# Kernel optimization log

Measured on AMD Instinct MI355X. Metric: run time of the kernel, lower is better.

The kernel has to match this reference:

```python
import jax, jax.numpy as jnp
import numpy as np

B, N, E = 4, 8192, 65536
OBS, H, OUT, NOUT = 128, 256, 1024, 18


def setup_inputs() -> dict:
    key = jax.random.key(0)
    ks = jax.random.split(key, 8)
    nodes = jax.random.normal(ks[0], (B, N, OBS), dtype=jnp.float32)
    edges = jax.random.randint(ks[1], (B, 2, E), 0, N, dtype=jnp.int64)
    # Glorot-ish init for weights
    W0 = jax.random.normal(ks[2], (OBS, H), dtype=jnp.float32) / np.float32(np.sqrt(OBS))
    W1 = jax.random.normal(ks[3], (H, OUT), dtype=jnp.float32) / np.float32(np.sqrt(H))
    W_logit = jax.random.normal(ks[4], (OUT, NOUT), dtype=jnp.float32) / np.float32(np.sqrt(OUT))
    W_val = jax.random.normal(ks[5], (OUT, 1), dtype=jnp.float32) / np.float32(np.sqrt(OUT))
    return {
        "nodes": nodes, "edges": edges,
        "W0": W0, "b0": jnp.zeros((H,), jnp.float32),
        "W1": W1, "b1": jnp.zeros((OUT,), jnp.float32),
        "W_logit": W_logit, "b_logit": jnp.zeros((NOUT,), jnp.float32),
        "W_val": W_val, "b_val": jnp.zeros((1,), jnp.float32),
    }


def _gcn_layer(x, src, dst, W, b, n):
    # PyG GCNConv: out = D^{-1/2} (A + I) D^{-1/2} X W + b   (self-loops already in src/dst)
    h = x @ W                                                     # [N, F_out]
    deg = jax.ops.segment_sum(jnp.ones(src.shape, jnp.float32), dst, num_segments=n)
    dinv = jnp.where(deg > 0, jax.lax.rsqrt(deg), 0.0)            # deg^{-1/2}
    norm = dinv[src] * dinv[dst]                                  # [Etot]
    msg = h[src] * norm[:, None]                                  # gather + normalize
    agg = jax.ops.segment_sum(msg, dst, num_segments=n)           # scatter-add
    return agg + b


def reference(nodes, edges, W0, b0, W1, b1, W_logit, b_logit, W_val, b_val):
    n = nodes.shape[1]
    loops = jnp.arange(n, dtype=edges.dtype)  # self-loops, added by GCNConv

    def per_graph(x, ei):
        src = jnp.concatenate([ei[0], loops])
        dst = jnp.concatenate([ei[1], loops])
        h = jax.nn.relu(_gcn_layer(x, src, dst, W0, b0, n))
        # (original applies F.dropout here; omitted for a deterministic reference)
        h = jax.nn.relu(_gcn_layer(h, src, dst, W1, b1, n))
        return h

    out = jax.vmap(per_graph)(nodes, edges)        # [B, N, OUT]
    logits = out @ W_logit + b_logit               # [B, N, NOUT]
    values = (out @ W_val + b_val)[..., 0]         # [B, N]
    return logits, values
```

## Files before the change

kernel.cpp:

```cpp
#include <hip/hip_runtime.h>
#include <hip/hip_bf16.h>

#define BB   4
#define NN   8192
#define EE   65536
#define FOBS 128
#define FH   256
#define FOUT 1024
#define NLOG 18
#define BKT  64

typedef __attribute__((ext_vector_type(8))) short frag8;
typedef __attribute__((ext_vector_type(4))) float f32x4;

__device__ __forceinline__ ushort f2b(float v) {
    __hip_bfloat16 h = __float2bfloat16(v);
    return *reinterpret_cast<ushort*>(&h);
}
__device__ __forceinline__ float blo(uint u) { return __uint_as_float(u << 16); }
__device__ __forceinline__ float bhi(uint u) { return __uint_as_float(u & 0xffff0000u); }

__device__ __forceinline__ void gld16(const void* g, void* l) {
    __builtin_amdgcn_global_load_lds(
        (const __attribute__((address_space(1))) unsigned*)g,
        (__attribute__((address_space(3))) unsigned*)l, 16, 0, 0);
}

#define W0_N   (FOBS * FH)
#define W1_N   (FH * FOUT)
#define WH_N   (19 * FOUT)
#define CUR_N  (BB * NN)
#define OUTI_N (BB * NN * 19)
#define PREP_TOTAL (W0_N + W1_N + WH_N + CUR_N + OUTI_N)

__global__ void prep_kernel(const float* __restrict__ W0, ushort* __restrict__ W0T,
                            const float* __restrict__ W1, ushort* __restrict__ W1T,
                            const float* __restrict__ Wl, const float* __restrict__ Wv,
                            ushort* __restrict__ WT19, int* __restrict__ cursor,
                            const float* __restrict__ bl, const float* __restrict__ bv,
                            float* __restrict__ out_logits, float* __restrict__ out_values) {
    int idx = blockIdx.x * blockDim.x + threadIdx.x;
    if (idx < W0_N) {
        int n = idx / FOBS, k = idx - n * FOBS;
        W0T[idx] = f2b(W0[(size_t)k * FH + n]);
        return;
    }
    idx -= W0_N;
    if (idx < W1_N) {
        int n = idx / FH, k = idx - n * FH;
        W1T[idx] = f2b(W1[(size_t)k * FOUT + n]);
        return;
    }
    idx -= W1_N;
    if (idx < WH_N) {
        int o = idx >> 10, k = idx & (FOUT - 1);
        WT19[idx] = f2b((o < NLOG) ? Wl[(size_t)k * NLOG + o] : Wv[k]);
        return;
    }
    idx -= WH_N;
    if (idx < CUR_N) { cursor[idx] = 0; return; }
    idx -= CUR_N;
    if (idx < OUTI_N) {
        int gn = idx / 19, o = idx - gn * 19;
        if (o < NLOG) out_logits[(size_t)gn * NLOG + o] = bl[o];
        else          out_values[gn] = bv[0];
    }
}

__global__ void bucket_fill(const int* __restrict__ edges, int* __restrict__ cursor,
                            int* __restrict__ bucket) {
    int blk = blockIdx.x;
    int xcd = blk & 7;
    int g = xcd >> 1;
    int chunk = (blk >> 3) * 2 + (xcd & 1);
    int e = chunk * 256 + threadIdx.x;
    const int* src = edges + (size_t)g * 2 * EE;
    const int* dst = src + EE;
    int d = dst[e];
    int slot = atomicAdd(&cursor[(size_t)g * NN + d], 1);
    if (slot < BKT) bucket[((size_t)g * NN + d) * BKT + slot] = src[e];
}

__global__ __launch_bounds__(256) void gather_agg_f32(
    const float* __restrict__ x_all, const int* __restrict__ cnt_all,
    const int* __restrict__ bucket, uint* __restrict__ agg_all)
{
    int blk = blockIdx.x;
    int xcd = blk & 7;
    int g = xcd >> 1;
    int chunk = (blk >> 3) * 2 + (xcd & 1);
    int wv = threadIdx.x >> 6, lane = threadIdx.x & 63;
    int n = chunk * 4 + wv;
    const float2* x = (const float2*)(x_all + (size_t)g * NN * FOBS);
    const int* cnt = cnt_all + (size_t)g * NN;
    const int* bkt = bucket + ((size_t)g * NN + n) * BKT;

    int cn = cnt[n];
    float wn = rsqrtf((float)cn + 1.0f);
    int deg = min(cn, BKT);

    float2 self = x[(size_t)n * 64 + lane];
    float ax = wn * wn * self.x, ay = wn * wn * self.y;

    for (int i = 0; i < deg; i += 8) {
        int last = deg - 1;
        int s0 = bkt[i];
        int s1 = bkt[min(i + 1, last)], s2 = bkt[min(i + 2, last)], s3 = bkt[min(i + 3, last)];
        int s4 = bkt[min(i + 4, last)], s5 = bkt[min(i + 5, last)], s6 = bkt[min(i + 6, last)];
        int s7 = bkt[min(i + 7, last)];
        float w0 = rsqrtf((float)cnt[s0] + 1.0f) * wn;
        float w1 = (i + 1 < deg) ? rsqrtf((float)cnt[s1] + 1.0f) * wn : 0.0f;
        float w2 = (i + 2 < deg) ? rsqrtf((float)cnt[s2] + 1.0f) * wn : 0.0f;
        float w3 = (i + 3 < deg) ? rsqrtf((float)cnt[s3] + 1.0f) * wn : 0.0f;
        float w4 = (i + 4 < deg) ? rsqrtf((float)cnt[s4] + 1.0f) * wn : 0.0f;
        float w5 = (i + 5 < deg) ? rsqrtf((float)cnt[s5] + 1.0f) * wn : 0.0f;
        float w6 = (i + 6 < deg) ? rsqrtf((float)cnt[s6] + 1.0f) * wn : 0.0f;
        float w7 = (i + 7 < deg) ? rsqrtf((float)cnt[s7] + 1.0f) * wn : 0.0f;
        float2 r0 = x[(size_t)s0 * 64 + lane], r1 = x[(size_t)s1 * 64 + lane];
        float2 r2 = x[(size_t)s2 * 64 + lane], r3 = x[(size_t)s3 * 64 + lane];
        float2 r4 = x[(size_t)s4 * 64 + lane], r5 = x[(size_t)s5 * 64 + lane];
        float2 r6 = x[(size_t)s6 * 64 + lane], r7 = x[(size_t)s7 * 64 + lane];
        ax += w0 * r0.x + w1 * r1.x + w2 * r2.x + w3 * r3.x
            + w4 * r4.x + w5 * r5.x + w6 * r6.x + w7 * r7.x;
        ay += w0 * r0.y + w1 * r1.y + w2 * r2.y + w3 * r3.y
            + w4 * r4.y + w5 * r5.y + w6 * r6.y + w7 * r7.y;
    }
    agg_all[((size_t)g * NN + n) * 64 + lane] = (uint)f2b(ax) | ((uint)f2b(ay) << 16);
}

__global__ __launch_bounds__(256) void gather_agg_b256(
    const uint2* __restrict__ xb_all, const int* __restrict__ cnt_all,
    const int* __restrict__ bucket, uint2* __restrict__ agg_all)
{
    int blk = blockIdx.x;
    int xcd = blk & 7;
    int g = xcd >> 1;
    int chunk = (blk >> 3) * 2 + (xcd & 1);
    int wv = threadIdx.x >> 6, lane = threadIdx.x & 63;
    int n = chunk * 4 + wv;
    const uint2* xb = xb_all + (size_t)g * NN * 64;
    const int* cnt = cnt_all + (size_t)g * NN;
    const int* bkt = bucket + ((size_t)g * NN + n) * BKT;

    int cn = cnt[n];
    float wn = rsqrtf((float)cn + 1.0f);
    int deg = min(cn, BKT);

    uint2 u = xb[(size_t)n * 64 + lane];
    float w2s = wn * wn;
    float a0 = w2s * blo(u.x), a1 = w2s * bhi(u.x), a2 = w2s * blo(u.y), a3 = w2s * bhi(u.y);

    for (int i = 0; i < deg; i += 8) {
        int last = deg - 1;
        int s0 = bkt[i];
        int s1 = bkt[min(i + 1, last)], s2 = bkt[min(i + 2, last)], s3 = bkt[min(i + 3, last)];
        int s4 = bkt[min(i + 4, last)], s5 = bkt[min(i + 5, last)], s6 = bkt[min(i + 6, last)];
        int s7 = bkt[min(i + 7, last)];
        float w0 = rsqrtf((float)cnt[s0] + 1.0f) * wn;
        float w1 = (i + 1 < deg) ? rsqrtf((float)cnt[s1] + 1.0f) * wn : 0.0f;
        float w2 = (i + 2 < deg) ? rsqrtf((float)cnt[s2] + 1.0f) * wn : 0.0f;
        float w3 = (i + 3 < deg) ? rsqrtf((float)cnt[s3] + 1.0f) * wn : 0.0f;
        float w4 = (i + 4 < deg) ? rsqrtf((float)cnt[s4] + 1.0f) * wn : 0.0f;
        float w5 = (i + 5 < deg) ? rsqrtf((float)cnt[s5] + 1.0f) * wn : 0.0f;
        float w6 = (i + 6 < deg) ? rsqrtf((float)cnt[s6] + 1.0f) * wn : 0.0f;
        float w7 = (i + 7 < deg) ? rsqrtf((float)cnt[s7] + 1.0f) * wn : 0.0f;
        uint2 r0 = xb[(size_t)s0 * 64 + lane], r1 = xb[(size_t)s1 * 64 + lane];
        uint2 r2 = xb[(size_t)s2 * 64 + lane], r3 = xb[(size_t)s3 * 64 + lane];
        uint2 r4 = xb[(size_t)s4 * 64 + lane], r5 = xb[(size_t)s5 * 64 + lane];
        uint2 r6 = xb[(size_t)s6 * 64 + lane], r7 = xb[(size_t)s7 * 64 + lane];
        a0 += w0 * blo(r0.x) + w1 * blo(r1.x) + w2 * blo(r2.x) + w3 * blo(r3.x)
            + w4 * blo(r4.x) + w5 * blo(r5.x) + w6 * blo(r6.x) + w7 * blo(r7.x);
        a1 += w0 * bhi(r0.x) + w1 * bhi(r1.x) + w2 * bhi(r2.x) + w3 * bhi(r3.x)
            + w4 * bhi(r4.x) + w5 * bhi(r5.x) + w6 * bhi(r6.x) + w7 * bhi(r7.x);
        a2 += w0 * blo(r0.y) + w1 * blo(r1.y) + w2 * blo(r2.y) + w3 * blo(r3.y)
            + w4 * blo(r4.y) + w5 * blo(r5.y) + w6 * blo(r6.y) + w7 * blo(r7.y);
        a3 += w0 * bhi(r0.y) + w1 * bhi(r1.y) + w2 * bhi(r2.y) + w3 * bhi(r3.y)
            + w4 * bhi(r4.y) + w5 * bhi(r5.y) + w6 * bhi(r6.y) + w7 * bhi(r7.y);
    }
    uint2 o;
    o.x = (uint)f2b(a0) | ((uint)f2b(a1) << 16);
    o.y = (uint)f2b(a2) | ((uint)f2b(a3) << 16);
    agg_all[((size_t)g * NN + n) * 64 + lane] = o;
}

__global__ __launch_bounds__(256) void mfma_gemm(
    const ushort* __restrict__ A_all, const ushort* __restrict__ BT,
    const float* __restrict__ bias, ushort* __restrict__ C_all,
    int M, int N, int K, int relu)
{
    __shared__ __align__(16) ushort As[128 * 64];
    __shared__ __align__(16) ushort Bs[128 * 64];

    int g = blockIdx.z;
    const ushort* A = A_all + (size_t)g * M * K;
    ushort* C = C_all + (size_t)g * M * N;

    int t = threadIdx.x;
    int bn = blockIdx.x, bm = blockIdx.y;
    int lane = t & 63, w = t >> 6;
    int wm = w >> 1, wn = w & 1;
    int l15 = lane & 15, quad = lane >> 4;

    f32x4 acc[4][4] = {};

    const char* Abase = (const char*)(A + (size_t)(bm * 128) * K);
    const char* Bbase = (const char*)(BT + (size_t)(bn * 128) * K);
    size_t rstride = (size_t)K * 2;

    int rsub = lane >> 3;
    int colb = (lane & 7) * 16;

    for (int k0 = 0; k0 < K; k0 += 64) {
#pragma unroll
        for (int c = 0; c < 4; ++c) {
            int grp = c * 4 + w;
            int row = grp * 8 + rsub;
            int gcol = k0 * 2 + (colb ^ ((row & 7) << 4));
            gld16(Abase + (size_t)row * rstride + gcol, (char*)As + grp * 1024);
            gld16(Bbase + (size_t)row * rstride + gcol, (char*)Bs + grp * 1024);
        }
        __syncthreads();
#pragma unroll
        for (int kk = 0; kk < 64; kk += 32) {
            frag8 af[4], bf[4];
#pragma unroll
            for (int i = 0; i < 4; ++i) {
                int r = wm * 64 + i * 16 + l15;
                int cb = (kk * 2 + quad * 16) ^ ((r & 7) << 4);
                af[i] = *(const frag8*)((const char*)As + r * 128 + cb);
            }
#pragma unroll
            for (int j = 0; j < 4; ++j) {
                int r = wn * 64 + j * 16 + l15;
                int cb = (kk * 2 + quad * 16) ^ ((r & 7) << 4);
                bf[j] = *(const frag8*)((const char*)Bs + r * 128 + cb);
            }
#pragma unroll
            for (int i = 0; i < 4; ++i)
#pragma unroll
                for (int j = 0; j < 4; ++j)
                    acc[i][j] = __builtin_amdgcn_mfma_f32_16x16x32_bf16(af[i], bf[j], acc[i][j], 0, 0, 0);
        }
        __syncthreads();
    }

#pragma unroll
    for (int i = 0; i < 4; ++i) {
#pragma unroll
        for (int j = 0; j < 4; ++j) {
            int col = bn * 128 + wn * 64 + j * 16 + l15;
            float bcol = bias[col];
#pragma unroll
            for (int r = 0; r < 4; ++r) {
                int row = bm * 128 + wm * 64 + i * 16 + quad * 4 + r;
                float v = acc[i][j][r] + bcol;
                if (relu) v = fmaxf(v, 0.0f);
                C[(size_t)row * N + col] = f2b(v);
            }
        }
    }
}

__global__ __launch_bounds__(256) void gemm2_heads(
    const ushort* __restrict__ hagg_all,
    const ushort* __restrict__ W1T,
    const float*  __restrict__ b1,
    const ushort* __restrict__ WT19,
    float* __restrict__ out_logits,
    float* __restrict__ out_values)
{
    __shared__ __align__(16) ushort smem[128 * 136];
    __shared__ __align__(16) ushort wt[20][136];

    char* AsB = (char*)smem;
    char* BsB = (char*)smem + 16384;
    ushort* Ct = smem;

    int bm = blockIdx.x, sp = blockIdx.y, g = blockIdx.z;
    int t = threadIdx.x;
    int lane = t & 63, w = t >> 6;
    int wm = w >> 1, wn = w & 1;
    int l15 = lane & 15, quad = lane >> 4;

    const char* A0 = (const char*)(hagg_all + ((size_t)g * NN + bm * 128) * FH);

    if (t < 136) wt[19][t] = 0;

    int rsub = lane >> 3;
    int colb = (lane & 7) * 16;

    f32x4 hacc[2][2] = {};

    for (int bi = 0; bi < 4; ++bi) {
        int bn = sp * 4 + bi;
        __syncthreads();

        for (int idx = t; idx < 19 * 16; idx += 256) {
            int row = idx >> 4, c8 = (idx & 15) * 8;
            *(uint4*)&wt[row][c8] = *(const uint4*)(WT19 + (size_t)row * FOUT + bn * 128 + c8);
        }

        f32x4 acc[4][4] = {};
        const char* Bbase = (const char*)(W1T + (size_t)(bn * 128) * FH);

        for (int k0 = 0; k0 < FH; k0 += 64) {
#pragma unroll
            for (int c = 0; c < 4; ++c) {
                int grp = c * 4 + w;
                int row = grp * 8 + rsub;
                int gcol = k0 * 2 + (colb ^ ((row & 7) << 4));
                gld16(A0 + (size_t)row * (FH * 2) + gcol, AsB + grp * 1024);
                gld16(Bbase + (size_t)row * (FH * 2) + gcol, BsB + grp * 1024);
            }
            __syncthreads();
#pragma unroll
            for (int kk = 0; kk < 64; kk += 32) {
                frag8 af[4], bf[4];
#pragma unroll
                for (int i = 0; i < 4; ++i) {
                    int r = wm * 64 + i * 16 + l15;
                    int cb = (kk * 2 + quad * 16) ^ ((r & 7) << 4);
                    af[i] = *(const frag8*)(AsB + r * 128 + cb);
                }
#pragma unroll
                for (int j = 0; j < 4; ++j) {
                    int r = wn * 64 + j * 16 + l15;
                    int cb = (kk * 2 + quad * 16) ^ ((r & 7) << 4);
                    bf[j] = *(const frag8*)(BsB + r * 128 + cb);
                }
#pragma unroll
                for (int i = 0; i < 4; ++i)
#pragma unroll
                    for (int j = 0; j < 4; ++j)
                        acc[i][j] = __builtin_amdgcn_mfma_f32_16x16x32_bf16(af[i], bf[j], acc[i][j], 0, 0, 0);
            }
            __syncthreads();
        }

#pragma unroll
        for (int j = 0; j < 4; ++j) {
            int colL = wn * 64 + j * 16 + l15;
            float bcol = b1[bn * 128 + colL];
#pragma unroll
            for (int i = 0; i < 4; ++i) {
                int rowL = wm * 64 + i * 16 + quad * 4;
#pragma unroll
                for (int r = 0; r < 4; ++r) {
                    float v = fmaxf(acc[i][j][r] + bcol, 0.0f);
                    Ct[(size_t)(rowL + r) * 136 + colL] = f2b(v);
                }
            }
        }
        __syncthreads();

        int r1 = (l15 < 3) ? (16 + l15) : 19;
#pragma unroll
        for (int kk = 0; kk < 128; kk += 32) {
            frag8 b0 = *(const frag8*)&wt[l15][kk + quad * 8];
            frag8 bO = *(const frag8*)&wt[r1][kk + quad * 8];
#pragma unroll
            for (int mt = 0; mt < 2; ++mt) {
                int row = (w * 2 + mt) * 16 + l15;
                frag8 af = *(const frag8*)&Ct[(size_t)row * 136 + kk + quad * 8];
                hacc[mt][0] = __builtin_amdgcn_mfma_f32_16x16x32_bf16(af, b0, hacc[mt][0], 0, 0, 0);
                hacc[mt][1] = __builtin_amdgcn_mfma_f32_16x16x32_bf16(af, bO, hacc[mt][1], 0, 0, 0);
            }
        }
    }

#pragma unroll
    for (int mt = 0; mt < 2; ++mt) {
#pragma unroll
        for (int r = 0; r < 4; ++r) {
            int node = bm * 128 + (w * 2 + mt) * 16 + quad * 4 + r;
            size_t gn = (size_t)g * NN + node;
            atomicAdd(&out_logits[gn * NLOG + l15], hacc[mt][0][r]);
            if (l15 < 2)       atomicAdd(&out_logits[gn * NLOG + 16 + l15], hacc[mt][1][r]);
            else if (l15 == 2) atomicAdd(&out_values[gn], hacc[mt][1][r]);
        }
    }
}

extern "C" void kernel_launch(void* const* d_in, const int* in_sizes, int n_in,
                              void* d_out, int out_size, void* d_ws, size_t ws_size,
                              hipStream_t stream) {
    const float* nodes = (const float*)d_in[0];
    const int*   edges = (const int*)d_in[1];
    const float* W0 = (const float*)d_in[2];
    const float* b0 = (const float*)d_in[3];
    const float* W1 = (const float*)d_in[4];
    const float* b1 = (const float*)d_in[5];
    const float* Wl = (const float*)d_in[6];
    const float* bl = (const float*)d_in[7];
    const float* Wv = (const float*)d_in[8];
    const float* bv = (const float*)d_in[9];

    float* out_logits = (float*)d_out;
    float* out_values = out_logits + (size_t)BB * NN * NLOG;

    char* ws = (char*)d_ws;
    int*    cursor  = (int*)(ws);
    ushort* W0T     = (ushort*)(ws + (128 << 10));
    ushort* W1T     = (ushort*)(ws + (192 << 10));
    ushort* WT19    = (ushort*)(ws + (704 << 10));
    int*    bucket  = (int*)(ws + (1u << 20));
    ushort* xagg_b  = (ushort*)(ws + (9u << 20));
    ushort* h1b     = (ushort*)(ws + (17u << 20));
    ushort* hagg_b  = (ushort*)(ws + (33u << 20));

    prep_kernel<<<(PREP_TOTAL + 255) / 256, 256, 0, stream>>>(
        W0, W0T, W1, W1T, Wl, Wv, WT19, cursor, bl, bv, out_logits, out_values);

    bucket_fill<<<1024, 256, 0, stream>>>(edges, cursor, bucket);

    gather_agg_f32<<<(NN / 4) * BB, 256, 0, stream>>>(nodes, cursor, bucket, (uint*)xagg_b);

    mfma_gemm<<<dim3(FH / 128, NN / 128, BB), 256, 0, stream>>>(
        xagg_b, W0T, b0, h1b, NN, FH, FOBS, 1);

    gather_agg_b256<<<(NN / 4) * BB, 256, 0, stream>>>((const uint2*)h1b, cursor, bucket,
                                                       (uint2*)hagg_b);

    gemm2_heads<<<dim3(NN / 128, 2, BB), 256, 0, stream>>>(hagg_b, W1T, b1, WT19,
                                                           out_logits, out_values);
}
```

Measured before the change: 187.5 us.

## Restructure head GEMM to full-width blocks with resident A panel and direct stores

The fused GEMM2+heads kernel now runs one 512-thread block per 128-row tile covering all 1024 output columns. It keeps the whole A panel in LDS and double-buffers W1 tiles, prefetching the next one while the current one is used. Because each block owns its rows completely, head outputs are written directly with bias added, replacing atomicAdd and the bias pre-initialisation in the prep kernel. The gather kernels also load bucket indices as two int4 vectors instead of eight scalar loads. In exchange the grid is halved, and the larger LDS footprint (about 135 KB) likely allows only one block per CU.

```diff
diff --git a/kernel.cpp b/kernel.cpp
--- a/kernel.cpp
+++ b/kernel.cpp
@@ -30,15 +30,12 @@
 #define W1_N   (FH * FOUT)
 #define WH_N   (19 * FOUT)
 #define CUR_N  (BB * NN)
-#define OUTI_N (BB * NN * 19)
-#define PREP_TOTAL (W0_N + W1_N + WH_N + CUR_N + OUTI_N)
+#define PREP_TOTAL (W0_N + W1_N + WH_N + CUR_N)
 
 __global__ void prep_kernel(const float* __restrict__ W0, ushort* __restrict__ W0T,
                             const float* __restrict__ W1, ushort* __restrict__ W1T,
                             const float* __restrict__ Wl, const float* __restrict__ Wv,
-                            ushort* __restrict__ WT19, int* __restrict__ cursor,
-                            const float* __restrict__ bl, const float* __restrict__ bv,
-                            float* __restrict__ out_logits, float* __restrict__ out_values) {
+                            ushort* __restrict__ WT19, int* __restrict__ cursor) {
     int idx = blockIdx.x * blockDim.x + threadIdx.x;
     if (idx < W0_N) {
         int n = idx / FOBS, k = idx - n * FOBS;
@@ -58,13 +55,7 @@
         return;
     }
     idx -= WH_N;
-    if (idx < CUR_N) { cursor[idx] = 0; return; }
-    idx -= CUR_N;
-    if (idx < OUTI_N) {
-        int gn = idx / 19, o = idx - gn * 19;
-        if (o < NLOG) out_logits[(size_t)gn * NLOG + o] = bl[o];
-        else          out_values[gn] = bv[0];
-    }
+    if (idx < CUR_N) cursor[idx] = 0;
 }
 
 __global__ void bucket_fill(const int* __restrict__ edges, int* __restrict__ cursor,
@@ -103,11 +94,16 @@
     float ax = wn * wn * self.x, ay = wn * wn * self.y;
 
     for (int i = 0; i < deg; i += 8) {
-        int last = deg - 1;
-        int s0 = bkt[i];
-        int s1 = bkt[min(i + 1, last)], s2 = bkt[min(i + 2, last)], s3 = bkt[min(i + 3, last)];
-        int s4 = bkt[min(i + 4, last)], s5 = bkt[min(i + 5, last)], s6 = bkt[min(i + 6, last)];
-        int s7 = bkt[min(i + 7, last)];
+        int4 va = *(const int4*)&bkt[i];
+        int4 vb = *(const int4*)&bkt[i + 4];
+        int s0 = va.x;
+        int s1 = (i + 1 < deg) ? va.y : s0;
+        int s2 = (i + 2 < deg) ? va.z : s0;
+        int s3 = (i + 3 < deg) ? va.w : s0;
+        int s4 = (i + 4 < deg) ? vb.x : s0;
+        int s5 = (i + 5 < deg) ? vb.y : s0;
+        int s6 = (i + 6 < deg) ? vb.z : s0;
+        int s7 = (i + 7 < deg) ? vb.w : s0;
         float w0 = rsqrtf((float)cnt[s0] + 1.0f) * wn;
         float w1 = (i + 1 < deg) ? rsqrtf((float)cnt[s1] + 1.0f) * wn : 0.0f;
         float w2 = (i + 2 < deg) ? rsqrtf((float)cnt[s2] + 1.0f) * wn : 0.0f;
@@ -151,11 +147,16 @@
     float a0 = w2s * blo(u.x), a1 = w2s * bhi(u.x), a2 = w2s * blo(u.y), a3 = w2s * bhi(u.y);
 
     for (int i = 0; i < deg; i += 8) {
-        int last = deg - 1;
-        int s0 = bkt[i];
-        int s1 = bkt[min(i + 1, last)], s2 = bkt[min(i + 2, last)], s3 = bkt[min(i + 3, last)];
-        int s4 = bkt[min(i + 4, last)], s5 = bkt[min(i + 5, last)], s6 = bkt[min(i + 6, last)];
-        int s7 = bkt[min(i + 7, last)];
+        int4 va = *(const int4*)&bkt[i];
+        int4 vb = *(const int4*)&bkt[i + 4];
+        int s0 = va.x;
+        int s1 = (i + 1 < deg) ? va.y : s0;
+        int s2 = (i + 2 < deg) ? va.z : s0;
+        int s3 = (i + 3 < deg) ? va.w : s0;
+        int s4 = (i + 4 < deg) ? vb.x : s0;
+        int s5 = (i + 5 < deg) ? vb.y : s0;
+        int s6 = (i + 6 < deg) ? vb.z : s0;
+        int s7 = (i + 7 < deg) ? vb.w : s0;
         float w0 = rsqrtf((float)cnt[s0] + 1.0f) * wn;
         float w1 = (i + 1 < deg) ? rsqrtf((float)cnt[s1] + 1.0f) * wn : 0.0f;
         float w2 = (i + 2 < deg) ? rsqrtf((float)cnt[s2] + 1.0f) * wn : 0.0f;
@@ -261,85 +262,103 @@
     }
 }
 
-__global__ __launch_bounds__(256) void gemm2_heads(
+__global__ __launch_bounds__(512) void gemm2_heads(
     const ushort* __restrict__ hagg_all,
     const ushort* __restrict__ W1T,
     const float*  __restrict__ b1,
     const ushort* __restrict__ WT19,
+    const float*  __restrict__ bl,
+    const float*  __restrict__ bv,
     float* __restrict__ out_logits,
     float* __restrict__ out_values)
 {
-    __shared__ __align__(16) ushort smem[128 * 136];
+    __shared__ __align__(16) char Apan[4][16384];
+    __shared__ __align__(16) char BsD[2][16384];
+    __shared__ __align__(16) ushort Ct[128 * 136];
     __shared__ __align__(16) ushort wt[20][136];
 
-    char* AsB = (char*)smem;
-    char* BsB = (char*)smem + 16384;
-    ushort* Ct = smem;
-
-    int bm = blockIdx.x, sp = blockIdx.y, g = blockIdx.z;
+    int bm = blockIdx.x, g = blockIdx.y;
     int t = threadIdx.x;
     int lane = t & 63, w = t >> 6;
-    int wm = w >> 1, wn = w & 1;
+    int wm = w >> 2, wn = w & 3;
     int l15 = lane & 15, quad = lane >> 4;
-
-    const char* A0 = (const char*)(hagg_all + ((size_t)g * NN + bm * 128) * FH);
-
-    if (t < 136) wt[19][t] = 0;
-
     int rsub = lane >> 3;
     int colb = (lane & 7) * 16;
 
-    f32x4 hacc[2][2] = {};
-
-    for (int bi = 0; bi < 4; ++bi) {
-        int bn = sp * 4 + bi;
-        __syncthreads();
-
-        for (int idx = t; idx < 19 * 16; idx += 256) {
-            int row = idx >> 4, c8 = (idx & 15) * 8;
-            *(uint4*)&wt[row][c8] = *(const uint4*)(WT19 + (size_t)row * FOUT + bn * 128 + c8);
-        }
-
-        f32x4 acc[4][4] = {};
-        const char* Bbase = (const char*)(W1T + (size_t)(bn * 128) * FH);
-
-        for (int k0 = 0; k0 < FH; k0 += 64) {
-#pragma unroll
-            for (int c = 0; c < 4; ++c) {
-                int grp = c * 4 + w;
-                int row = grp * 8 + rsub;
-                int gcol = k0 * 2 + (colb ^ ((row & 7) << 4));
-                gld16(A0 + (size_t)row * (FH * 2) + gcol, AsB + grp * 1024);
-                gld16(Bbase + (size_t)row * (FH * 2) + gcol, BsB + grp * 1024);
-            }
-            __syncthreads();
+    const char* A0 = (const char*)(hagg_all + ((size_t)g * NN + bm * 128) * FH);
+
+#pragma unroll
+    for (int cc = 0; cc < 8; ++cc) {
+        int grp = cc * 8 + w;
+        int chunk = grp >> 4, gi = grp & 15;
+        int row = gi * 8 + rsub;
+        int gcol = chunk * 128 + (colb ^ ((row & 7) << 4));
+        gld16(A0 + (size_t)row * (FH * 2) + gcol, Apan[chunk] + gi * 1024);
+    }
+#pragma unroll
+    for (int c = 0; c < 2; ++c) {
+        int grp = c * 8 + w;
+        int row = grp * 8 + rsub;
+        int gcol = colb ^ ((row & 7) << 4);
+        gld16((const char*)W1T + (size_t)row * (FH * 2) + gcol, BsD[0] + grp * 1024);
+    }
+    if (t < 136) wt[19][t] = 0;
+    __syncthreads();
+
+    f32x4 hacc[2] = {};
+
+    for (int bn = 0; bn < 8; ++bn) {
+        f32x4 acc[4][2] = {};
+#pragma unroll
+        for (int k0i = 0; k0i < 4; ++k0i) {
+            int s = bn * 4 + k0i;
+            if (s < 31) {
+                int ns = s + 1;
+                int nbn = ns >> 2, nk = ns & 3;
+                const char* Bb = (const char*)(W1T + (size_t)(nbn * 128) * FH);
+#pragma unroll
+                for (int c = 0; c < 2; ++c) {
+                    int grp = c * 8 + w;
+                    int row = grp * 8 + rsub;
+                    int gcol = nk * 128 + (colb ^ ((row & 7) << 4));
+                    gld16(Bb + (size_t)row * (FH * 2) + gcol, BsD[ns & 1] + grp * 1024);
+                }
+            }
+            if (k0i == 0) {
+                for (int idx = t; idx < 19 * 16; idx += 512) {
+                    int row = idx >> 4, c8 = (idx & 15) * 8;
+                    *(uint4*)&wt[row][c8] = *(const uint4*)(WT19 + (size_t)row * FOUT + bn * 128 + c8);
+                }
+            }
+            const char* Bs = BsD[s & 1];
+            const char* Ap = Apan[k0i];
 #pragma unroll
             for (int kk = 0; kk < 64; kk += 32) {
-                frag8 af[4], bf[4];
+                frag8 af[4], bf[2];
 #pragma unroll
                 for (int i = 0; i < 4; ++i) {
                     int r = wm * 64 + i * 16 + l15;
                     int cb = (kk * 2 + quad * 16) ^ ((r & 7) << 4);
-                    af[i] = *(const frag8*)(AsB + r * 128 + cb);
+                    af[i] = *(const frag8*)(Ap + r * 128 + cb);
                 }
 #pragma unroll
-                for (int j = 0; j < 4; ++j) {
-                    int r = wn * 64 + j * 16 + l15;
+                for (int j = 0; j < 2; ++j) {
+                    int r = wn * 32 + j * 16 + l15;
                     int cb = (kk * 2 + quad * 16) ^ ((r & 7) << 4);
-                    bf[j] = *(const frag8*)(BsB + r * 128 + cb);
+                    bf[j] = *(const frag8*)(Bs + r * 128 + cb);
                 }
 #pragma unroll
                 for (int i = 0; i < 4; ++i)
 #pragma unroll
-                    for (int j = 0; j < 4; ++j)
+                    for (int j = 0; j < 2; ++j)
                         acc[i][j] = __builtin_amdgcn_mfma_f32_16x16x32_bf16(af[i], bf[j], acc[i][j], 0, 0, 0);
             }
             __syncthreads();
         }
 
 #pragma unroll
-        for (int j = 0; j < 4; ++j) {
-            int colL = wn * 64 + j * 16 + l15;
+        for (int j = 0; j < 2; ++j) {
+            int colL = wn * 32 + j * 16 + l15;
             float bcol = b1[bn * 128 + colL];
 #pragma unroll
             for (int i = 0; i < 4; ++i) {
@@ -358,26 +377,20 @@
         for (int kk = 0; kk < 128; kk += 32) {
             frag8 b0 = *(const frag8*)&wt[l15][kk + quad * 8];
             frag8 bO = *(const frag8*)&wt[r1][kk + quad * 8];
-#pragma unroll
-            for (int mt = 0; mt < 2; ++mt) {
-                int row = (w * 2 + mt) * 16 + l15;
-                frag8 af = *(const frag8*)&Ct[(size_t)row * 136 + kk + quad * 8];
-                hacc[mt][0] = __builtin_amdgcn_mfma_f32_16x16x32_bf16(af, b0, hacc[mt][0], 0, 0, 0);
-                hacc[mt][1] = __builtin_amdgcn_mfma_f32_16x16x32_bf16(af, bO, hacc[mt][1], 0, 0, 0);
-            }
-        }
-    }
-
-#pragma unroll
-    for (int mt = 0; mt < 2; ++mt) {
-#pragma unroll
-        for (int r = 0; r < 4; ++r) {
-            int node = bm * 128 + (w * 2 + mt) * 16 + quad * 4 + r;
-            size_t gn = (size_t)g * NN + node;
-            atomicAdd(&out_logits[gn * NLOG + l15], hacc[mt][0][r]);
-            if (l15 < 2)       atomicAdd(&out_logits[gn * NLOG + 16 + l15], hacc[mt][1][r]);
-            else if (l15 == 2) atomicAdd(&out_values[gn], hacc[mt][1][r]);
-        }
+            frag8 af = *(const frag8*)&Ct[(size_t)(w * 16 + l15) * 136 + kk + quad * 8];
+            hacc[0] = __builtin_amdgcn_mfma_f32_16x16x32_bf16(af, b0, hacc[0], 0, 0, 0);
+            hacc[1] = __builtin_amdgcn_mfma_f32_16x16x32_bf16(af, bO, hacc[1], 0, 0, 0);
+        }
+        __syncthreads();
+    }
+
+#pragma unroll
+    for (int r = 0; r < 4; ++r) {
+        int node = bm * 128 + w * 16 + quad * 4 + r;
+        size_t gn = (size_t)g * NN + node;
+        out_logits[gn * NLOG + l15] = hacc[0][r] + bl[l15];
+        if (l15 < 2)       out_logits[gn * NLOG + 16 + l15] = hacc[1][r] + bl[16 + l15];
+        else if (l15 == 2) out_values[gn] = hacc[1][r] + bv[0];
     }
 }
 
@@ -409,7 +422,7 @@
     ushort* hagg_b  = (ushort*)(ws + (33u << 20));
 
     prep_kernel<<<(PREP_TOTAL + 255) / 256, 256, 0, stream>>>(
-        W0, W0T, W1, W1T, Wl, Wv, WT19, cursor, bl, bv, out_logits, out_values);
+        W0, W0T, W1, W1T, Wl, Wv, WT19, cursor);
 
     bucket_fill<<<1024, 256, 0, stream>>>(edges, cursor, bucket);
 
@@ -421,6 +434,6 @@
     gather_agg_b256<<<(NN / 4) * BB, 256, 0, stream>>>((const uint2*)h1b, cursor, bucket,
                                                        (uint2*)hagg_b);
 
-    gemm2_heads<<<dim3(NN / 128, 2, BB), 256, 0, stream>>>(hagg_b, W1T, b1, WT19,
-                                                           out_logits, out_values);
-}
+    gemm2_heads<<<dim3(NN / 128, BB), 512, 0, stream>>>(hagg_b, W1T, b1, WT19, bl, bv,
+                                                        out_logits, out_values);
+}
```

Measured after the change: 189.7 us. Within noise of the previous version (+1.2%).

## Pre-convert node features to bf16 and store bucket indices as 16-bit

Applied to the files above, without the earlier changes.

The prep kernel now converts the fp32 node features to packed bf16, so the first gather reads half as many bytes per neighbour row. Bucket entries are stored as ushort instead of int, and both gather kernels load eight indices with one 16-byte vector load. This cuts gather traffic and index loads, at the cost of an extra full pass over the nodes in prep and bf16 rounding of the layer-1 inputs. The vector index load reads past deg, but stays inside the fixed 64-slot bucket.

```diff
diff --git a/kernel.cpp b/kernel.cpp
--- a/kernel.cpp
+++ b/kernel.cpp
@@ -26,20 +26,28 @@
         (__attribute__((address_space(3))) unsigned*)l, 16, 0, 0);
 }
 
+#define XB2_N  (BB * NN * FOBS / 2)
 #define W0_N   (FOBS * FH)
 #define W1_N   (FH * FOUT)
 #define WH_N   (19 * FOUT)
 #define CUR_N  (BB * NN)
 #define OUTI_N (BB * NN * 19)
-#define PREP_TOTAL (W0_N + W1_N + WH_N + CUR_N + OUTI_N)
-
-__global__ void prep_kernel(const float* __restrict__ W0, ushort* __restrict__ W0T,
+#define PREP_TOTAL (XB2_N + W0_N + W1_N + WH_N + CUR_N + OUTI_N)
+
+__global__ void prep_kernel(const float* __restrict__ nodes, uint* __restrict__ xb,
+                            const float* __restrict__ W0, ushort* __restrict__ W0T,
                             const float* __restrict__ W1, ushort* __restrict__ W1T,
                             const float* __restrict__ Wl, const float* __restrict__ Wv,
                             ushort* __restrict__ WT19, int* __restrict__ cursor,
                             const float* __restrict__ bl, const float* __restrict__ bv,
                             float* __restrict__ out_logits, float* __restrict__ out_values) {
     int idx = blockIdx.x * blockDim.x + threadIdx.x;
+    if (idx < XB2_N) {
+        float2 xx = ((const float2*)nodes)[idx];
+        xb[idx] = (uint)f2b(xx.x) | ((uint)f2b(xx.y) << 16);
+        return;
+    }
+    idx -= XB2_N;
     if (idx < W0_N) {
         int n = idx / FOBS, k = idx - n * FOBS;
         W0T[idx] = f2b(W0[(size_t)k * FH + n]);
@@ -68,7 +76,7 @@
 }
 
 __global__ void bucket_fill(const int* __restrict__ edges, int* __restrict__ cursor,
-                            int* __restrict__ bucket) {
+                            ushort* __restrict__ bucket) {
     int blk = blockIdx.x;
     int xcd = blk & 7;
     int g = xcd >> 1;
@@ -78,12 +86,12 @@
     const int* dst = src + EE;
     int d = dst[e];
     int slot = atomicAdd(&cursor[(size_t)g * NN + d], 1);
-    if (slot < BKT) bucket[((size_t)g * NN + d) * BKT + slot] = src[e];
-}
-
-__global__ __launch_bounds__(256) void gather_agg_f32(
-    const float* __restrict__ x_all, const int* __restrict__ cnt_all,
-    const int* __restrict__ bucket, uint* __restrict__ agg_all)
+    if (slot < BKT) bucket[((size_t)g * NN + d) * BKT + slot] = (ushort)src[e];
+}
+
+__global__ __launch_bounds__(256) void gather_agg_b128(
+    const uint* __restrict__ xb_all, const int* __restrict__ cnt_all,
+    const ushort* __restrict__ bucket, uint* __restrict__ agg_all)
 {
     int blk = blockIdx.x;
     int xcd = blk & 7;
@@ -91,23 +99,28 @@
     int chunk = (blk >> 3) * 2 + (xcd & 1);
     int wv = threadIdx.x >> 6, lane = threadIdx.x & 63;
     int n = chunk * 4 + wv;
-    const float2* x = (const float2*)(x_all + (size_t)g * NN * FOBS);
+    const uint* xb = xb_all + (size_t)g * NN * 64;
     const int* cnt = cnt_all + (size_t)g * NN;
-    const int* bkt = bucket + ((size_t)g * NN + n) * BKT;
+    const ushort* bkt = bucket + ((size_t)g * NN + n) * BKT;
 
     int cn = cnt[n];
     float wn = rsqrtf((float)cn + 1.0f);
     int deg = min(cn, BKT);
 
-    float2 self = x[(size_t)n * 64 + lane];
-    float ax = wn * wn * self.x, ay = wn * wn * self.y;
+    uint u = xb[(size_t)n * 64 + lane];
+    float w2s = wn * wn;
+    float a0 = w2s * blo(u), a1 = w2s * bhi(u);
 
     for (int i = 0; i < deg; i += 8) {
-        int last = deg - 1;
-        int s0 = bkt[i];
-        int s1 = bkt[min(i + 1, last)], s2 = bkt[min(i + 2, last)], s3 = bkt[min(i + 3, last)];
-        int s4 = bkt[min(i + 4, last)], s5 = bkt[min(i + 5, last)], s6 = bkt[min(i + 6, last)];
-        int s7 = bkt[min(i + 7, last)];
+        uint4 va = *(const uint4*)&bkt[i];
+        int s0 = (int)(va.x & 0xffffu);
+        int s1 = (i + 1 < deg) ? (int)(va.x >> 16) : s0;
+        int s2 = (i + 2 < deg) ? (int)(va.y & 0xffffu) : s0;
+        int s3 = (i + 3 < deg) ? (int)(va.y >> 16) : s0;
+        int s4 = (i + 4 < deg) ? (int)(va.z & 0xffffu) : s0;
+        int s5 = (i + 5 < deg) ? (int)(va.z >> 16) : s0;
+        int s6 = (i + 6 < deg) ? (int)(va.w & 0xffffu) : s0;
+        int s7 = (i + 7 < deg) ? (int)(va.w >> 16) : s0;
         float w0 = rsqrtf((float)cnt[s0] + 1.0f) * wn;
         float w1 = (i + 1 < deg) ? rsqrtf((float)cnt[s1] + 1.0f) * wn : 0.0f;
         float w2 = (i + 2 < deg) ? rsqrtf((float)cnt[s2] + 1.0f) * wn : 0.0f;
@@ -116,21 +129,21 @@
         float w5 = (i + 5 < deg) ? rsqrtf((float)cnt[s5] + 1.0f) * wn : 0.0f;
         float w6 = (i + 6 < deg) ? rsqrtf((float)cnt[s6] + 1.0f) * wn : 0.0f;
         float w7 = (i + 7 < deg) ? rsqrtf((float)cnt[s7] + 1.0f) * wn : 0.0f;
-        float2 r0 = x[(size_t)s0 * 64 + lane], r1 = x[(size_t)s1 * 64 + lane];
-        float2 r2 = x[(size_t)s2 * 64 + lane], r3 = x[(size_t)s3 * 64 + lane];
-        float2 r4 = x[(size_t)s4 * 64 + lane], r5 = x[(size_t)s5 * 64 + lane];
-        float2 r6 = x[(size_t)s6 * 64 + lane], r7 = x[(size_t)s7 * 64 + lane];
-        ax += w0 * r0.x + w1 * r1.x + w2 * r2.x + w3 * r3.x
-            + w4 * r4.x + w5 * r5.x + w6 * r6.x + w7 * r7.x;
-        ay += w0 * r0.y + w1 * r1.y + w2 * r2.y + w3 * r3.y
-            + w4 * r4.y + w5 * r5.y + w6 * r6.y + w7 * r7.y;
-    }
-    agg_all[((size_t)g * NN + n) * 64 + lane] = (uint)f2b(ax) | ((uint)f2b(ay) << 16);
+        uint r0 = xb[(size_t)s0 * 64 + lane], r1 = xb[(size_t)s1 * 64 + lane];
+        uint r2 = xb[(size_t)s2 * 64 + lane], r3 = xb[(size_t)s3 * 64 + lane];
+        uint r4 = xb[(size_t)s4 * 64 + lane], r5 = xb[(size_t)s5 * 64 + lane];
+        uint r6 = xb[(size_t)s6 * 64 + lane], r7 = xb[(size_t)s7 * 64 + lane];
+        a0 += w0 * blo(r0) + w1 * blo(r1) + w2 * blo(r2) + w3 * blo(r3)
+            + w4 * blo(r4) + w5 * blo(r5) + w6 * blo(r6) + w7 * blo(r7);
+        a1 += w0 * bhi(r0) + w1 * bhi(r1) + w2 * bhi(r2) + w3 * bhi(r3)
+            + w4 * bhi(r4) + w5 * bhi(r5) + w6 * bhi(r6) + w7 * bhi(r7);
+    }
+    agg_all[((size_t)g * NN + n) * 64 + lane] = (uint)f2b(a0) | ((uint)f2b(a1) << 16);
 }
 
 __global__ __launch_bounds__(256) void gather_agg_b256(
     const uint2* __restrict__ xb_all, const int* __restrict__ cnt_all,
-    const int* __restrict__ bucket, uint2* __restrict__ agg_all)
+    const ushort* __restrict__ bucket, uint2* __restrict__ agg_all)
 {
     int blk = blockIdx.x;
     int xcd = blk & 7;
@@ -140,7 +153,7 @@
     int n = chunk * 4 + wv;
     const uint2* xb = xb_all + (size_t)g * NN * 64;
     const int* cnt = cnt_all + (size_t)g * NN;
-    const int* bkt = bucket + ((size_t)g * NN + n) * BKT;
+    const ushort* bkt = bucket + ((size_t)g * NN + n) * BKT;
 
     int cn = cnt[n];
     float wn = rsqrtf((float)cn + 1.0f);
@@ -151,11 +164,15 @@
     float a0 = w2s * blo(u.x), a1 = w2s * bhi(u.x), a2 = w2s * blo(u.y), a3 = w2s * bhi(u.y);
 
     for (int i = 0; i < deg; i += 8) {
-        int last = deg - 1;
-        int s0 = bkt[i];
-        int s1 = bkt[min(i + 1, last)], s2 = bkt[min(i + 2, last)], s3 = bkt[min(i + 3, last)];
-        int s4 = bkt[min(i + 4, last)], s5 = bkt[min(i + 5, last)], s6 = bkt[min(i + 6, last)];
-        int s7 = bkt[min(i + 7, last)];
+        uint4 va = *(const uint4*)&bkt[i];
+        int s0 = (int)(va.x & 0xffffu);
+        int s1 = (i + 1 < deg) ? (int)(va.x >> 16) : s0;
+        int s2 = (i + 2 < deg) ? (int)(va.y & 0xffffu) : s0;
+        int s3 = (i + 3 < deg) ? (int)(va.y >> 16) : s0;
+        int s4 = (i + 4 < deg) ? (int)(va.z & 0xffffu) : s0;
+        int s5 = (i + 5 < deg) ? (int)(va.z >> 16) : s0;
+        int s6 = (i + 6 < deg) ? (int)(va.w & 0xffffu) : s0;
+        int s7 = (i + 7 < deg) ? (int)(va.w >> 16) : s0;
         float w0 = rsqrtf((float)cnt[s0] + 1.0f) * wn;
         float w1 = (i + 1 < deg) ? rsqrtf((float)cnt[s1] + 1.0f) * wn : 0.0f;
         float w2 = (i + 2 < deg) ? rsqrtf((float)cnt[s2] + 1.0f) * wn : 0.0f;
@@ -403,17 +420,18 @@
     ushort* W0T     = (ushort*)(ws + (128 << 10));
     ushort* W1T     = (ushort*)(ws + (192 << 10));
     ushort* WT19    = (ushort*)(ws + (704 << 10));
-    int*    bucket  = (int*)(ws + (1u << 20));
-    ushort* xagg_b  = (ushort*)(ws + (9u << 20));
-    ushort* h1b     = (ushort*)(ws + (17u << 20));
-    ushort* hagg_b  = (ushort*)(ws + (33u << 20));
+    uint*   xb      = (uint*)(ws + (1u << 20));
+    ushort* bucket  = (ushort*)(ws + (9u << 20));
+    ushort* xagg_b  = (ushort*)(ws + (13u << 20));
+    ushort* h1b     = (ushort*)(ws + (21u << 20));
+    ushort* hagg_b  = (ushort*)(ws + (37u << 20));
 
     prep_kernel<<<(PREP_TOTAL + 255) / 256, 256, 0, stream>>>(
-        W0, W0T, W1, W1T, Wl, Wv, WT19, cursor, bl, bv, out_logits, out_values);
+        nodes, xb, W0, W0T, W1, W1T, Wl, Wv, WT19, cursor, bl, bv, out_logits, out_values);
 
     bucket_fill<<<1024, 256, 0, stream>>>(edges, cursor, bucket);
 
-    gather_agg_f32<<<(NN / 4) * BB, 256, 0, stream>>>(nodes, cursor, bucket, (uint*)xagg_b);
+    gather_agg_b128<<<(NN / 4) * BB, 256, 0, stream>>>(xb, cursor, bucket, (uint*)xagg_b);
 
     mfma_gemm<<<dim3(FH / 128, NN / 128, BB), 256, 0, stream>>>(
         xagg_b, W0T, b0, h1b, NN, FH, FOBS, 1);
```

Result: no change. 185.9 us (-0.8%).
